# Kernel tuning notes

Hardware: AMD Instinct MI355X
Metric: run time of the kernel (lower is better)

Reference implementation:

```python
import jax, jax.numpy as jnp
import numpy as np

B, H, S, D = 4, 16, 2048, 64
SCALE = 8.0  # sqrt(D)
NEG = -1000000000.0


def setup_inputs() -> dict:
    key = jax.random.key(0)
    kq, kk, kv = jax.random.split(key, 3)
    q = jax.random.normal(kq, (B, H, S, D), dtype=jnp.float32)
    k = jax.random.normal(kk, (B, H, S, D), dtype=jnp.float32)
    v = jax.random.normal(kv, (B, H, S, D), dtype=jnp.float32)
    # causal mask: True means masked out (matches torch masked_fill)
    mask = jnp.triu(jnp.ones((S, S), dtype=bool), k=1)[None, None, :, :]
    mask = jnp.broadcast_to(mask, (B, 1, S, S))
    return {"q": q, "k": k, "v": v, "mask": mask}


def reference(q, k, v, mask):
    # score = q @ k^T / scale  -> [B,H,S,S]
    score = jnp.einsum("bhqd,bhkd->bhqk", q, k) / SCALE
    score = jnp.where(mask, NEG, score)
    probs = jax.nn.softmax(score, axis=-1)
    context = jnp.einsum("bhqk,bhkd->bhqd", probs, v)
    return context
```

## Files before the change

kernel.cpp:

```cpp
#include <hip/hip_runtime.h>

#define SQ 2048
#define DH 64
#define BK 64
#define NQT 32
#define NBH 64
#define M0 8.0f

#define WS_BYTES ((size_t)2 * NBH * SQ * DH * 2)

typedef float f32x4 __attribute__((ext_vector_type(4)));
typedef __bf16 bf16x8 __attribute__((ext_vector_type(8)));
typedef _Float16 f16x4 __attribute__((ext_vector_type(4)));
typedef _Float16 f16x8 __attribute__((ext_vector_type(8)));
typedef __fp16 fp16x2 __attribute__((ext_vector_type(2)));
typedef unsigned short u16x8 __attribute__((ext_vector_type(8)));
typedef unsigned int u32x4 __attribute__((ext_vector_type(4)));

static __device__ __forceinline__ unsigned int pkbf(float a, float b) {
#if __has_builtin(__builtin_amdgcn_cvt_pk_bf16_f32)
  typedef __bf16 bf16x2 __attribute__((ext_vector_type(2)));
  bf16x2 r = __builtin_amdgcn_cvt_pk_bf16_f32(a, b);
  return __builtin_bit_cast(unsigned int, r);
#else
  unsigned int ua = __builtin_bit_cast(unsigned int, a);
  unsigned int ub = __builtin_bit_cast(unsigned int, b);
  ua += 0x7fffu + ((ua >> 16) & 1u);
  ub += 0x7fffu + ((ub >> 16) & 1u);
  return (ua >> 16) | (ub & 0xffff0000u);
#endif
}

static __device__ __forceinline__ unsigned int pkf16(float a, float b) {
  fp16x2 r = __builtin_amdgcn_cvt_pkrtz(a, b);
  return __builtin_bit_cast(unsigned int, r);
}

static __device__ __forceinline__ f32x4 mfma_qk(u16x8 a, u16x8 b, f32x4 c) {
  return __builtin_amdgcn_mfma_f32_16x16x32_bf16(
      __builtin_bit_cast(bf16x8, a), __builtin_bit_cast(bf16x8, b), c, 0, 0, 0);
}

static __device__ __forceinline__ f32x4 mfma_pv(f16x4 a, f16x4 b, f32x4 c) {
  return __builtin_amdgcn_mfma_f32_16x16x16f16(a, b, c, 0, 0, 0);
}

static __device__ __forceinline__ f32x4 mfma_pv32(f16x8 a, f16x8 b, f32x4 c) {
  return __builtin_amdgcn_mfma_f32_16x16x32_f16(a, b, c, 0, 0, 0);
}

static __device__ __forceinline__ void ld16(unsigned short* l, const unsigned short* g) {
  __builtin_amdgcn_global_load_lds(
      (const __attribute__((address_space(1))) unsigned int*)(const void*)g,
      (__attribute__((address_space(3))) unsigned int*)(void*)l, 16, 0, 0);
}

static __device__ __forceinline__ void store_tile(float* wb, float* dst,
                                                  const f32x4* o, int lane,
                                                  int l15, int quad) {
#pragma unroll
  for (int dt = 0; dt < 4; ++dt) {
    const int colw = dt * 16 + quad * 4;
    *(f32x4*)&wb[l15 * 64 + (colw ^ ((l15 & 3) * 16))] = o[dt];
  }
  __builtin_amdgcn_wave_barrier();
#pragma unroll
  for (int j = 0; j < 4; ++j) {
    const int row = j * 4 + (lane >> 4);
    const int colw = (lane & 15) * 4;
    f32x4 v = *(const f32x4*)&wb[row * 64 + (colw ^ ((row & 3) * 16))];
    *(f32x4*)&dst[row * 64 + colw] = v;
  }
}

__global__ __launch_bounds__(256) void prep(const float* __restrict__ K,
                                            const float* __restrict__ V,
                                            unsigned short* __restrict__ Kb,
                                            unsigned short* __restrict__ Vt) {
  const int bh = (int)blockIdx.x >> 5;
  const int st = (int)blockIdx.x & 31;
  const int tid = threadIdx.x;
  __shared__ __align__(16) unsigned short T[DH * 64];
  {
    const int r = tid >> 2, c0 = (tid & 3) * 16;
    const float* kp = K + ((size_t)bh * SQ + st * 64 + r) * DH + c0;
    f32x4 x0 = *(const f32x4*)kp, x1 = *(const f32x4*)(kp + 4),
          x2 = *(const f32x4*)(kp + 8), x3 = *(const f32x4*)(kp + 12);
    u32x4 w0 = {pkbf(x0[0], x0[1]), pkbf(x0[2], x0[3]), pkbf(x1[0], x1[1]), pkbf(x1[2], x1[3])};
    u32x4 w1 = {pkbf(x2[0], x2[1]), pkbf(x2[2], x2[3]), pkbf(x3[0], x3[1]), pkbf(x3[2], x3[3])};
    unsigned short* kb = Kb + ((size_t)bh * SQ + st * 64 + r) * DH + c0;
    *(u32x4*)kb = w0;
    *(u32x4*)(kb + 8) = w1;
  }
  {
    const int kvb = (tid >> 4) * 4, vdb = (tid & 15) * 4;
    const float* vp = V + ((size_t)bh * SQ + st * 64 + kvb) * DH + vdb;
    f32x4 r0 = *(const f32x4*)vp, r1 = *(const f32x4*)(vp + DH),
          r2 = *(const f32x4*)(vp + 2 * DH), r3 = *(const f32x4*)(vp + 3 * DH);
    const int uu = kvb >> 3, h = (kvb >> 2) & 1;
#pragma unroll
    for (int i = 0; i < 4; ++i) {
      const int d = vdb + i;
      uint2 w = {pkf16(r0[i], r1[i]), pkf16(r2[i], r3[i])};
      *(uint2*)&T[d * 64 + ((uu ^ (d & 7)) * 8) + h * 4] = w;
    }
  }
  __syncthreads();
  {
    const int d2 = tid >> 2, cp = (tid & 3) * 2;
#pragma unroll
    for (int e = 0; e < 2; ++e) {
      const int uu = cp + e;
      u16x8 val = *(const u16x8*)&T[d2 * 64 + ((uu ^ (d2 & 7)) * 8)];
      *(u16x8*)&Vt[(size_t)bh * DH * SQ + (size_t)d2 * SQ + st * 64 + uu * 8] = val;
    }
  }
}

__global__ __launch_bounds__(256, 4) void fa_main(
    const float* __restrict__ Q, const unsigned short* __restrict__ Kb,
    const unsigned short* __restrict__ Vt, float* __restrict__ O) {
  const int lin = (int)blockIdx.x;
  const int xcd = lin & 7, u = lin >> 3;
  const int hh = u & 7;
  const int pi = (int)((0x32104567BA98CDEFull >> ((u >> 3) * 4)) & 15u);
  const int bh = hh * 8 + xcd;
  const int tend = 2 * pi + 1;

  const int tid = threadIdx.x;
  const int wv = tid >> 6;
  const int lane = tid & 63;
  const int l15 = lane & 15;
  const int quad = lane >> 4;

  __shared__ __align__(16) unsigned short S0[2 * BK * DH];
  __shared__ __align__(16) unsigned short S1[2 * BK * DH];

  const size_t hq = (size_t)bh * (SQ * DH);
  const unsigned short* KbH = Kb + (size_t)bh * SQ * DH;
  const unsigned short* VtH = Vt + (size_t)bh * DH * SQ;

  const int srow = wv * 16 + (lane >> 3);
  const int sc = lane & 7;

  const int qbase = pi * 128 + wv * 32;
  const int dtw = 2 * pi + (wv >> 1);
  const int qo = (wv & 1) * 32;

  u16x8 qf[2][2];
  {
    const float scq = 0.125f * 1.4426950408889634f;
#pragma unroll
    for (int f = 0; f < 2; ++f) {
      const float* qp = Q + hq + (size_t)(qbase + 16 * f + l15) * DH + quad * 8;
#pragma unroll
      for (int c = 0; c < 2; ++c) {
        f32x4 x = *(const f32x4*)(qp + c * 32);
        f32x4 y = *(const f32x4*)(qp + c * 32 + 4);
        u32x4 w = {pkbf(x[0] * scq, x[1] * scq), pkbf(x[2] * scq, x[3] * scq),
                   pkbf(y[0] * scq, y[1] * scq), pkbf(y[2] * scq, y[3] * scq)};
        qf[f][c] = __builtin_bit_cast(u16x8, w);
      }
    }
  }

  f32x4 o0[4], o1[4], la0, la1;
#pragma unroll
  for (int dt = 0; dt < 4; ++dt) {
    o0[dt] = (f32x4){0.f, 0.f, 0.f, 0.f};
    o1[dt] = (f32x4){0.f, 0.f, 0.f, 0.f};
  }
  la0 = (f32x4){0.f, 0.f, 0.f, 0.f};
  la1 = (f32x4){0.f, 0.f, 0.f, 0.f};
  const f16x8 ones8 = {(_Float16)1.f, (_Float16)1.f, (_Float16)1.f, (_Float16)1.f,
                       (_Float16)1.f, (_Float16)1.f, (_Float16)1.f, (_Float16)1.f};

  auto stage = [&](unsigned short* W, int t) {
    const int kb = t * BK;
    unsigned short* Kd = W;
    unsigned short* Vd = W + BK * DH;
#pragma unroll
    for (int j = 0; j < 2; ++j) {
      const int p = srow + j * 8;
      const int kp = (p & ~31) | (((p >> 2) & 3) << 3) | (((p >> 4) & 1) << 2) | (p & 3);
      ld16(&Kd[p * 64 + sc * 8], &KbH[(size_t)(kb + kp) * 64 + ((sc ^ (p & 7)) * 8)]);
      ld16(&Vd[p * 64 + sc * 8], &VtH[(size_t)p * SQ + kb + ((sc ^ (p & 7)) * 8)]);
    }
  };

  auto attend = [&](const unsigned short* R, bool diag) {
    const unsigned short* Ks = R;
    const unsigned short* Vs = R + BK * DH;
    f32x4 s0[4], s1[4];
#pragma unroll
    for (int nt = 0; nt < 4; ++nt) {
      f32x4 a0 = {-M0, -M0, -M0, -M0}, a1 = {-M0, -M0, -M0, -M0};
#pragma unroll
      for (int c = 0; c < 2; ++c) {
        const int row = nt * 16 + l15;
        const int un = c * 4 + quad;
        u16x8 kf = *(const u16x8*)&Ks[row * 64 + ((un ^ (row & 7)) * 8)];
        a0 = mfma_qk(kf, qf[0][c], a0);
        a1 = mfma_qk(kf, qf[1][c], a1);
      }
      s0[nt] = a0;
      s1[nt] = a1;
    }
    if (diag) {
#pragma unroll
      for (int nt = 0; nt < 4; ++nt)
#pragma unroll
        for (int r = 0; r < 4; ++r) {
          const int kvl = (nt >> 1) * 32 + quad * 8 + (nt & 1) * 4 + r;
          if (kvl > qo + l15) s0[nt][r] = -1e30f;
          if (kvl > qo + 16 + l15) s1[nt][r] = -1e30f;
        }
    }
    f16x8 pf0[2], pf1[2];
#pragma unroll
    for (int n2 = 0; n2 < 2; ++n2) {
      f32x4 pe0, po0, pe1, po1;
#pragma unroll
      for (int r = 0; r < 4; ++r) {
        pe0[r] = __builtin_amdgcn_exp2f(s0[2 * n2][r]);
        po0[r] = __builtin_amdgcn_exp2f(s0[2 * n2 + 1][r]);
        pe1[r] = __builtin_amdgcn_exp2f(s1[2 * n2][r]);
        po1[r] = __builtin_amdgcn_exp2f(s1[2 * n2 + 1][r]);
      }
      u32x4 w0 = {pkf16(pe0[0], pe0[1]), pkf16(pe0[2], pe0[3]),
                  pkf16(po0[0], po0[1]), pkf16(po0[2], po0[3])};
      u32x4 w1 = {pkf16(pe1[0], pe1[1]), pkf16(pe1[2], pe1[3]),
                  pkf16(po1[0], po1[1]), pkf16(po1[2], po1[3])};
      pf0[n2] = __builtin_bit_cast(f16x8, w0);
      pf1[n2] = __builtin_bit_cast(f16x8, w1);
    }
#pragma unroll
    for (int n2 = 0; n2 < 2; ++n2) {
      la0 = mfma_pv32(ones8, pf0[n2], la0);
      la1 = mfma_pv32(ones8, pf1[n2], la1);
    }
#pragma unroll
    for (int dt = 0; dt < 4; ++dt) {
      const int d = dt * 16 + l15;
#pragma unroll
      for (int n2 = 0; n2 < 2; ++n2) {
        const int uv = n2 * 4 + quad;
        f16x8 vf = *(const f16x8*)&Vs[d * 64 + ((uv ^ (d & 7)) * 8)];
        o0[dt] = mfma_pv32(vf, pf0[n2], o0[dt]);
        o1[dt] = mfma_pv32(vf, pf1[n2], o1[dt]);
      }
    }
  };

  auto step = [&](int t, const unsigned short* R, unsigned short* W) {
    if (t <= dtw) attend(R, t == dtw);
    __syncthreads();
    if (t + 2 <= tend) stage(W, t + 2);
  };

  stage(S0, 0);
  __syncthreads();
  stage(S1, 1);
  for (int t = 0; t <= tend; t += 2) {
    step(t, S0, S0);
    if (t + 1 <= tend) step(t + 1, S1, S1);
  }

  float* wb = (float*)S0 + wv * 1024;
  {
    const float inv = 1.0f / la0[0];
    f32x4 on[4];
#pragma unroll
    for (int dt = 0; dt < 4; ++dt) on[dt] = o0[dt] * inv;
    store_tile(wb, O + hq + (size_t)(qbase)*DH, on, lane, l15, quad);
  }
  {
    const float inv = 1.0f / la1[0];
    f32x4 on[4];
#pragma unroll
    for (int dt = 0; dt < 4; ++dt) on[dt] = o1[dt] * inv;
    store_tile(wb, O + hq + (size_t)(qbase + 16) * DH, on, lane, l15, quad);
  }
}

__global__ __launch_bounds__(256, 4) void fa_full(
    const float* __restrict__ Q, const float* __restrict__ K,
    const float* __restrict__ V, float* __restrict__ O) {
  const int lin = (int)blockIdx.x;
  const int xcd = lin & 7;
  const int u = lin >> 3;
  const int hh = u & 7;
  const int p = u >> 3;
  const int bh = hh * 8 + xcd;
  const int tid = threadIdx.x;
  const int wv = tid >> 6;
  const int lane = tid & 63;
  const int l15 = lane & 15;
  const int quad = lane >> 4;
  __shared__ __align__(16) unsigned short SMEM[2][2 * BK * DH];
  const size_t hbase = (size_t)bh * (SQ * DH);
  const int krr = tid >> 3, kcc = (tid & 7) * 8;
  const int kvb = (tid >> 4) * 4, vdb = (tid & 15) * 4;
#pragma unroll
  for (int ph = 0; ph < 2; ++ph) {
    const int qt = ph ? (NQT - 1 - p) : p;
    const int wq0 = qt * 64 + wv * 16;
    u16x8 qf[2];
    {
      const float scq = 0.125f * 1.4426950408889634f;
      const float* qp = Q + hbase + (size_t)(wq0 + l15) * DH + quad * 8;
#pragma unroll
      for (int c = 0; c < 2; ++c) {
        f32x4 x = *(const f32x4*)(qp + c * 32);
        f32x4 y = *(const f32x4*)(qp + c * 32 + 4);
        u32x4 w = {pkbf(x[0] * scq, x[1] * scq), pkbf(x[2] * scq, x[3] * scq),
                   pkbf(y[0] * scq, y[1] * scq), pkbf(y[2] * scq, y[3] * scq)};
        qf[c] = __builtin_bit_cast(u16x8, w);
      }
    }
    f32x4 o[4];
#pragma unroll
    for (int dt = 0; dt < 4; ++dt) o[dt] = (f32x4){0.f, 0.f, 0.f, 0.f};
    float l = 0.f;
    f32x4 ka[2][2], va[4];
    {
      const float* kp = K + hbase + (size_t)krr * DH + kcc;
      ka[0][0] = *(const f32x4*)kp;             ka[0][1] = *(const f32x4*)(kp + 4);
      ka[1][0] = *(const f32x4*)(kp + 32 * DH); ka[1][1] = *(const f32x4*)(kp + 32 * DH + 4);
      const float* vp = V + hbase + (size_t)kvb * DH + vdb;
      va[0] = *(const f32x4*)vp;            va[1] = *(const f32x4*)(vp + DH);
      va[2] = *(const f32x4*)(vp + 2 * DH); va[3] = *(const f32x4*)(vp + 3 * DH);
    }
    __syncthreads();
    {
      unsigned short* Ksn = SMEM[0];
      unsigned short* Vsn = SMEM[0] + BK * DH;
#pragma unroll
      for (int h = 0; h < 2; ++h) {
        const int rr = h * 32 + krr;
        u32x4 w = {pkbf(ka[h][0][0], ka[h][0][1]), pkbf(ka[h][0][2], ka[h][0][3]),
                   pkbf(ka[h][1][0], ka[h][1][1]), pkbf(ka[h][1][2], ka[h][1][3])};
        *(u32x4*)&Ksn[rr * DH + (kcc ^ ((rr & 7) * 8))] = w;
      }
#pragma unroll
      for (int i = 0; i < 4; ++i) {
        const int d = vdb + i;
        uint2 w = {pkf16(va[0][i], va[1][i]), pkf16(va[2][i], va[3][i])};
        *(uint2*)&Vsn[d * BK + (kvb ^ ((d & 15) * 4))] = w;
      }
    }
    __syncthreads();
    for (int t = 0; t <= qt; ++t) {
      const unsigned short* Ks = SMEM[t & 1];
      const unsigned short* Vs = SMEM[t & 1] + BK * DH;
      if (t < qt) {
        const int kb2 = (t + 1) * BK;
        const float* kp = K + hbase + (size_t)(kb2 + krr) * DH + kcc;
        ka[0][0] = *(const f32x4*)kp;             ka[0][1] = *(const f32x4*)(kp + 4);
        ka[1][0] = *(const f32x4*)(kp + 32 * DH); ka[1][1] = *(const f32x4*)(kp + 32 * DH + 4);
        const float* vp = V + hbase + (size_t)(kb2 + kvb) * DH + vdb;
        va[0] = *(const f32x4*)vp;            va[1] = *(const f32x4*)(vp + DH);
        va[2] = *(const f32x4*)(vp + 2 * DH); va[3] = *(const f32x4*)(vp + 3 * DH);
      }
      f32x4 s[4];
#pragma unroll
      for (int nt = 0; nt < 4; ++nt) {
        f32x4 acc = {-M0, -M0, -M0, -M0};
#pragma unroll
        for (int c = 0; c < 2; ++c) {
          const int row = nt * 16 + l15;
          u16x8 kf = *(const u16x8*)&Ks[row * DH + ((c * 32 + quad * 8) ^ ((l15 & 7) * 8))];
          acc = mfma_qk(kf, qf[c], acc);
        }
        s[nt] = acc;
      }
      if (t == qt) {
#pragma unroll
        for (int nt = 0; nt < 4; ++nt)
#pragma unroll
          for (int r = 0; r < 4; ++r)
            if (nt * 16 + quad * 4 + r > wv * 16 + l15) s[nt][r] = -1e30f;
      }
      f16x4 pf[4];
#pragma unroll
      for (int nt = 0; nt < 4; ++nt) {
        f32x4 pr;
#pragma unroll
        for (int r = 0; r < 4; ++r) { pr[r] = __builtin_amdgcn_exp2f(s[nt][r]); l += pr[r]; }
        uint2 w2 = {pkf16(pr[0], pr[1]), pkf16(pr[2], pr[3])};
        pf[nt] = __builtin_bit_cast(f16x4, w2);
      }
#pragma unroll
      for (int dt = 0; dt < 4; ++dt) {
        const int d = dt * 16 + l15;
#pragma unroll
        for (int nt = 0; nt < 4; ++nt) {
          f16x4 vf = *(const f16x4*)&Vs[d * BK + ((nt * 16 + quad * 4) ^ (l15 * 4))];
          o[dt] = mfma_pv(vf, pf[nt], o[dt]);
        }
      }
      if (t < qt) {
        unsigned short* Ksn = SMEM[(t + 1) & 1];
        unsigned short* Vsn = SMEM[(t + 1) & 1] + BK * DH;
#pragma unroll
        for (int h = 0; h < 2; ++h) {
          const int rr = h * 32 + krr;
          u32x4 w = {pkbf(ka[h][0][0], ka[h][0][1]), pkbf(ka[h][0][2], ka[h][0][3]),
                     pkbf(ka[h][1][0], ka[h][1][1]), pkbf(ka[h][1][2], ka[h][1][3])};
          *(u32x4*)&Ksn[rr * DH + (kcc ^ ((rr & 7) * 8))] = w;
        }
#pragma unroll
        for (int i = 0; i < 4; ++i) {
          const int d = vdb + i;
          uint2 w = {pkf16(va[0][i], va[1][i]), pkf16(va[2][i], va[3][i])};
          *(uint2*)&Vsn[d * BK + (kvb ^ ((d & 15) * 4))] = w;
        }
        __syncthreads();
      }
    }
    l += __shfl_xor(l, 16, 64);
    l += __shfl_xor(l, 32, 64);
    const float inv = 1.0f / l;
    f32x4 on[4];
#pragma unroll
    for (int dt = 0; dt < 4; ++dt) on[dt] = o[dt] * inv;
    float* wb = (float*)SMEM[(qt + 1) & 1] + wv * 1024;
    store_tile(wb, O + hbase + (size_t)wq0 * DH, on, lane, l15, quad);
  }
}

extern "C" void kernel_launch(void* const* d_in, const int* in_sizes, int n_in,
                              void* d_out, int out_size, void* d_ws, size_t ws_size,
                              hipStream_t stream) {
  const float* q = (const float*)d_in[0];
  const float* k = (const float*)d_in[1];
  const float* v = (const float*)d_in[2];
  float* o = (float*)d_out;
  if (ws_size >= WS_BYTES) {
    unsigned short* Kb = (unsigned short*)d_ws;
    unsigned short* Vt = Kb + (size_t)NBH * SQ * DH;
    prep<<<dim3(NBH * 32), 256, 0, stream>>>(k, v, Kb, Vt);
    fa_main<<<dim3(1024), 256, 0, stream>>>(q, Kb, Vt, o);
  } else {
    fa_full<<<dim3(1024), 256, 0, stream>>>(q, k, v, o);
  }
}
```

Baseline: 202.6 us.

## Pre-swizzle K/V into MFMA fragment order and read V directly from global

The prep kernel now writes K and V tiles in the exact per-lane fragment order the MFMA instructions consume, so each lane does one contiguous 16-byte load per fragment. K is still staged through LDS, but with a linear copy and no XOR swizzle. V fragments are now loaded straight from global memory into registers inside attend, issued early to hide latency. This halves LDS traffic and footprint per stage and removes address arithmetic, at the cost of per-wave global reads of V that are repeated across the four waves and rely on cache hits.

```diff
diff --git a/kernel.cpp b/kernel.cpp
--- a/kernel.cpp
+++ b/kernel.cpp
@@ -75,23 +75,12 @@
 
 __global__ __launch_bounds__(256) void prep(const float* __restrict__ K,
                                             const float* __restrict__ V,
-                                            unsigned short* __restrict__ Kb,
-                                            unsigned short* __restrict__ Vt) {
+                                            unsigned short* __restrict__ Kf,
+                                            unsigned short* __restrict__ Vf) {
   const int bh = (int)blockIdx.x >> 5;
   const int st = (int)blockIdx.x & 31;
   const int tid = threadIdx.x;
   __shared__ __align__(16) unsigned short T[DH * 64];
-  {
-    const int r = tid >> 2, c0 = (tid & 3) * 16;
-    const float* kp = K + ((size_t)bh * SQ + st * 64 + r) * DH + c0;
-    f32x4 x0 = *(const f32x4*)kp, x1 = *(const f32x4*)(kp + 4),
-          x2 = *(const f32x4*)(kp + 8), x3 = *(const f32x4*)(kp + 12);
-    u32x4 w0 = {pkbf(x0[0], x0[1]), pkbf(x0[2], x0[3]), pkbf(x1[0], x1[1]), pkbf(x1[2], x1[3])};
-    u32x4 w1 = {pkbf(x2[0], x2[1]), pkbf(x2[2], x2[3]), pkbf(x3[0], x3[1]), pkbf(x3[2], x3[3])};
-    unsigned short* kb = Kb + ((size_t)bh * SQ + st * 64 + r) * DH + c0;
-    *(u32x4*)kb = w0;
-    *(u32x4*)(kb + 8) = w1;
-  }
   {
     const int kvb = (tid >> 4) * 4, vdb = (tid & 15) * 4;
     const float* vp = V + ((size_t)bh * SQ + st * 64 + kvb) * DH + vdb;
@@ -105,21 +94,37 @@
       *(uint2*)&T[d * 64 + ((uu ^ (d & 7)) * 8) + h * 4] = w;
     }
   }
+  {
+    const size_t kin = ((size_t)bh * SQ + st * 64) * DH;
+    unsigned short* kfo = Kf + (size_t)bh * SQ * DH + (size_t)st * 64 * DH;
+#pragma unroll
+    for (int e = 0; e < 2; ++e) {
+      const int L = tid * 2 + e;
+      const int l15 = L & 15, quad = (L >> 4) & 3, c = (L >> 6) & 1, nt = (L >> 7) & 3;
+      const int krow = (nt >> 1) * 32 + ((l15 >> 2) & 3) * 8 + (nt & 1) * 4 + (l15 & 3);
+      const float* kp = K + kin + (size_t)krow * DH + (c * 4 + quad) * 8;
+      f32x4 x = *(const f32x4*)kp, y = *(const f32x4*)(kp + 4);
+      u32x4 w = {pkbf(x[0], x[1]), pkbf(x[2], x[3]), pkbf(y[0], y[1]), pkbf(y[2], y[3])};
+      *(u32x4*)&kfo[L * 8] = w;
+    }
+  }
   __syncthreads();
   {
-    const int d2 = tid >> 2, cp = (tid & 3) * 2;
+    unsigned short* vfo = Vf + (size_t)bh * SQ * DH + (size_t)st * 64 * DH;
 #pragma unroll
     for (int e = 0; e < 2; ++e) {
-      const int uu = cp + e;
-      u16x8 val = *(const u16x8*)&T[d2 * 64 + ((uu ^ (d2 & 7)) * 8)];
-      *(u16x8*)&Vt[(size_t)bh * DH * SQ + (size_t)d2 * SQ + st * 64 + uu * 8] = val;
+      const int L = tid * 2 + e;
+      const int l15 = L & 15, quad = (L >> 4) & 3, dt = (L >> 6) & 3, n2 = (L >> 8) & 1;
+      const int d = dt * 16 + l15, uu = n2 * 4 + quad;
+      u16x8 val = *(const u16x8*)&T[d * 64 + ((uu ^ (d & 7)) * 8)];
+      *(u16x8*)&vfo[L * 8] = val;
     }
   }
 }
 
 __global__ __launch_bounds__(256, 4) void fa_main(
-    const float* __restrict__ Q, const unsigned short* __restrict__ Kb,
-    const unsigned short* __restrict__ Vt, float* __restrict__ O) {
+    const float* __restrict__ Q, const unsigned short* __restrict__ Kf,
+    const unsigned short* __restrict__ Vf, float* __restrict__ O) {
   const int lin = (int)blockIdx.x;
   const int xcd = lin & 7, u = lin >> 3;
   const int hh = u & 7;
@@ -133,15 +138,11 @@
   const int l15 = lane & 15;
   const int quad = lane >> 4;
 
-  __shared__ __align__(16) unsigned short S0[2 * BK * DH];
-  __shared__ __align__(16) unsigned short S1[2 * BK * DH];
+  __shared__ __align__(16) unsigned short SS[2][BK * DH];
 
   const size_t hq = (size_t)bh * (SQ * DH);
-  const unsigned short* KbH = Kb + (size_t)bh * SQ * DH;
-  const unsigned short* VtH = Vt + (size_t)bh * DH * SQ;
-
-  const int srow = wv * 16 + (lane >> 3);
-  const int sc = lane & 7;
+  const unsigned short* KfH = Kf + (size_t)bh * SQ * DH;
+  const unsigned short* VfH = Vf + (size_t)bh * SQ * DH;
 
   const int qbase = pi * 128 + wv * 32;
   const int dtw = 2 * pi + (wv >> 1);
@@ -176,30 +177,26 @@
                        (_Float16)1.f, (_Float16)1.f, (_Float16)1.f, (_Float16)1.f};
 
   auto stage = [&](unsigned short* W, int t) {
-    const int kb = t * BK;
-    unsigned short* Kd = W;
-    unsigned short* Vd = W + BK * DH;
 #pragma unroll
     for (int j = 0; j < 2; ++j) {
-      const int p = srow + j * 8;
-      const int kp = (p & ~31) | (((p >> 2) & 3) << 3) | (((p >> 4) & 1) << 2) | (p & 3);
-      ld16(&Kd[p * 64 + sc * 8], &KbH[(size_t)(kb + kp) * 64 + ((sc ^ (p & 7)) * 8)]);
-      ld16(&Vd[p * 64 + sc * 8], &VtH[(size_t)p * SQ + kb + ((sc ^ (p & 7)) * 8)]);
+      const int off = wv * 1024 + j * 512 + lane * 8;
+      ld16(&W[off], &KfH[(size_t)t * 4096 + off]);
     }
   };
 
-  auto attend = [&](const unsigned short* R, bool diag) {
-    const unsigned short* Ks = R;
-    const unsigned short* Vs = R + BK * DH;
+  auto attend = [&](const unsigned short* Ks, int t, bool diag) {
+    const unsigned short* vg = VfH + (size_t)t * 4096;
+    f16x8 vb0[4];
+#pragma unroll
+    for (int dt = 0; dt < 4; ++dt)
+      vb0[dt] = *(const f16x8*)&vg[(0 * 4 + dt) * 512 + lane * 8];
     f32x4 s0[4], s1[4];
 #pragma unroll
     for (int nt = 0; nt < 4; ++nt) {
       f32x4 a0 = {-M0, -M0, -M0, -M0}, a1 = {-M0, -M0, -M0, -M0};
 #pragma unroll
       for (int c = 0; c < 2; ++c) {
-        const int row = nt * 16 + l15;
-        const int un = c * 4 + quad;
-        u16x8 kf = *(const u16x8*)&Ks[row * 64 + ((un ^ (row & 7)) * 8)];
+        u16x8 kf = *(const u16x8*)&Ks[(nt * 2 + c) * 512 + lane * 8];
         a0 = mfma_qk(kf, qf[0][c], a0);
         a1 = mfma_qk(kf, qf[1][c], a1);
       }
@@ -234,39 +231,41 @@
       pf0[n2] = __builtin_bit_cast(f16x8, w0);
       pf1[n2] = __builtin_bit_cast(f16x8, w1);
     }
-#pragma unroll
-    for (int n2 = 0; n2 < 2; ++n2) {
-      la0 = mfma_pv32(ones8, pf0[n2], la0);
-      la1 = mfma_pv32(ones8, pf1[n2], la1);
-    }
+    f16x8 vb1[4];
+#pragma unroll
+    for (int dt = 0; dt < 4; ++dt)
+      vb1[dt] = *(const f16x8*)&vg[(1 * 4 + dt) * 512 + lane * 8];
+    la0 = mfma_pv32(ones8, pf0[0], la0);
+    la1 = mfma_pv32(ones8, pf1[0], la1);
+    la0 = mfma_pv32(ones8, pf0[1], la0);
+    la1 = mfma_pv32(ones8, pf1[1], la1);
 #pragma unroll
     for (int dt = 0; dt < 4; ++dt) {
-      const int d = dt * 16 + l15;
-#pragma unroll
-      for (int n2 = 0; n2 < 2; ++n2) {
-        const int uv = n2 * 4 + quad;
-        f16x8 vf = *(const f16x8*)&Vs[d * 64 + ((uv ^ (d & 7)) * 8)];
-        o0[dt] = mfma_pv32(vf, pf0[n2], o0[dt]);
-        o1[dt] = mfma_pv32(vf, pf1[n2], o1[dt]);
-      }
+      o0[dt] = mfma_pv32(vb0[dt], pf0[0], o0[dt]);
+      o1[dt] = mfma_pv32(vb0[dt], pf1[0], o1[dt]);
+    }
+#pragma unroll
+    for (int dt = 0; dt < 4; ++dt) {
+      o0[dt] = mfma_pv32(vb1[dt], pf0[1], o0[dt]);
+      o1[dt] = mfma_pv32(vb1[dt], pf1[1], o1[dt]);
     }
   };
 
   auto step = [&](int t, const unsigned short* R, unsigned short* W) {
-    if (t <= dtw) attend(R, t == dtw);
+    if (t <= dtw) attend(R, t, t == dtw);
     __syncthreads();
     if (t + 2 <= tend) stage(W, t + 2);
   };
 
-  stage(S0, 0);
+  stage(SS[0], 0);
   __syncthreads();
-  stage(S1, 1);
+  stage(SS[1], 1);
   for (int t = 0; t <= tend; t += 2) {
-    step(t, S0, S0);
-    if (t + 1 <= tend) step(t + 1, S1, S1);
-  }
-
-  float* wb = (float*)S0 + wv * 1024;
+    step(t, SS[0], SS[0]);
+    if (t + 1 <= tend) step(t + 1, SS[1], SS[1]);
+  }
+
+  float* wb = (float*)SS + wv * 1024;
   {
     const float inv = 1.0f / la0[0];
     f32x4 on[4];
@@ -437,10 +436,10 @@
   const float* v = (const float*)d_in[2];
   float* o = (float*)d_out;
   if (ws_size >= WS_BYTES) {
-    unsigned short* Kb = (unsigned short*)d_ws;
-    unsigned short* Vt = Kb + (size_t)NBH * SQ * DH;
-    prep<<<dim3(NBH * 32), 256, 0, stream>>>(k, v, Kb, Vt);
-    fa_main<<<dim3(1024), 256, 0, stream>>>(q, Kb, Vt, o);
+    unsigned short* Kf = (unsigned short*)d_ws;
+    unsigned short* Vf = Kf + (size_t)NBH * SQ * DH;
+    prep<<<dim3(NBH * 32), 256, 0, stream>>>(k, v, Kf, Vf);
+    fa_main<<<dim3(1024), 256, 0, stream>>>(q, Kf, Vf, o);
   } else {
     fa_full<<<dim3(1024), 256, 0, stream>>>(q, k, v, o);
   }
```

New measurement: 206.9 us. +2.1%, slower.
